# Kernel optimization log

Measured on AMD Instinct MI355X. Metric: run time of the kernel, lower is better.

## Reference

```python
import jax, jax.numpy as jnp
import numpy as np

DIM = 4096
N_HEADS = 32
N_KV = 8
HEAD_DIM = 128
WINDOW = 4096
BSZ = 1
SEQ = 2048
REPEATS = N_HEADS // N_KV
SCALE = HEAD_DIM ** -0.5
NEG_INF = -1e9


def setup_inputs() -> dict:
    key = jax.random.key(0)
    ks = jax.random.split(key, 5)
    x = jax.random.normal(ks[0], (1, BSZ, SEQ, DIM), jnp.float32)
    wq = jax.random.normal(ks[1], (N_HEADS * HEAD_DIM, DIM), jnp.float32) * (DIM ** -0.5)
    wk = jax.random.normal(ks[2], (N_KV * HEAD_DIM, DIM), jnp.float32) * (DIM ** -0.5)
    wv = jax.random.normal(ks[3], (N_KV * HEAD_DIM, DIM), jnp.float32) * (DIM ** -0.5)
    wo = jax.random.normal(ks[4], (DIM, N_HEADS * HEAD_DIM), jnp.float32) * (DIM ** -0.5)
    # rotary frequencies (Mistral/LLaMA style, base 10000)
    inv = 1.0 / (10000.0 ** (np.arange(0, HEAD_DIM, 2, dtype=np.float32) / HEAD_DIM))
    ang = np.outer(np.arange(SEQ, dtype=np.float32), inv)  # [SEQ, HEAD_DIM//2]
    freqs_cos = jnp.asarray(np.cos(ang), jnp.float32)
    freqs_sin = jnp.asarray(np.sin(ang), jnp.float32)
    positions = jnp.arange(SEQ, dtype=jnp.int32)
    # sliding-window causal additive mask [SEQ, SEQ]
    i = np.arange(SEQ)[:, None]
    j = np.arange(SEQ)[None, :]
    allowed = (j <= i) & (j > i - WINDOW)
    mask = jnp.asarray(np.where(allowed, 0.0, NEG_INF).astype(np.float32))
    cache_k = jnp.zeros((BSZ, WINDOW, N_KV, HEAD_DIM), jnp.float32)
    cache_v = jnp.zeros((BSZ, WINDOW, N_KV, HEAD_DIM), jnp.float32)
    return dict(x=x, wq=wq, wk=wk, wv=wv, wo=wo, freqs_cos=freqs_cos,
                freqs_sin=freqs_sin, positions=positions, mask=mask,
                cache_k=cache_k, cache_v=cache_v)


def _rope(x, cos, sin):
    # x: [b, s, h, hd]; pairs (x0,x1),(x2,x3),... treated as complex numbers
    xr = x[..., 0::2]
    xi = x[..., 1::2]
    c = cos[None, :, None, :]
    s = sin[None, :, None, :]
    out_r = xr * c - xi * s
    out_i = xr * s + xi * c
    return jnp.stack([out_r, out_i], axis=-1).reshape(x.shape)


def reference(x, wq, wk, wv, wo, freqs_cos, freqs_sin, positions, mask, cache_k, cache_v):
    b, s = BSZ, SEQ
    xf = x.reshape(b, s, DIM)
    xq = (xf @ wq.T).reshape(b, s, N_HEADS, HEAD_DIM)
    xk = (xf @ wk.T).reshape(b, s, N_KV, HEAD_DIM)
    xv = (xf @ wv.T).reshape(b, s, N_KV, HEAD_DIM)
    xq = _rope(xq, freqs_cos, freqs_sin)
    xk = _rope(xk, freqs_cos, freqs_sin)
    # sliding-window KV cache scatter update (last WINDOW positions, mod WINDOW)
    pos = positions[-WINDOW:] % WINDOW
    cache_k = cache_k.at[:, pos].set(xk[:, -WINDOW:])
    cache_v = cache_v.at[:, pos].set(xv[:, -WINDOW:])
    # prefill branch (positions.shape[0] > 1): attend over current xk/xv
    key = jnp.repeat(xk, REPEATS, axis=2)  # GQA repeat_kv -> [b, s, H, hd]
    val = jnp.repeat(xv, REPEATS, axis=2)
    q = xq.transpose(0, 2, 1, 3)  # [b, H, s, hd]
    k = key.transpose(0, 2, 1, 3)
    v = val.transpose(0, 2, 1, 3)
    scores = jnp.einsum('bhqd,bhkd->bhqk', q, k) * SCALE + mask[None, None]
    probs = jax.nn.softmax(scores, axis=-1)
    out = jnp.einsum('bhqk,bhkd->bhqd', probs, v)
    out = out.transpose(0, 2, 1, 3).reshape(1, b, s, N_HEADS * HEAD_DIM)
    return out @ wo.T, cache_k, cache_v
```

## Files before the change

### kernel.cpp

```cpp
#include <hip/hip_runtime.h>
#include <hip/hip_bf16.h>


typedef __attribute__((ext_vector_type(8))) short short8_t;
typedef __attribute__((ext_vector_type(2))) unsigned uint2_t;
typedef __attribute__((ext_vector_type(8))) __bf16 bf16x8;
typedef __attribute__((ext_vector_type(4))) float f32x4;
typedef __attribute__((ext_vector_type(16))) float f32x16;

#define SEQLEN 2048
#define QSCALE 0.08838834764831845f

__device__ __forceinline__ short f2b(float f) {
  if (!__builtin_isfinite(f)) f = 0.0f;
  union { float f; unsigned u; } v; v.f = f;
  unsigned r = (v.u + 0x7fffu + ((v.u >> 16) & 1u)) >> 16;
  return (short)r;
}
__device__ __forceinline__ float sf(float f) {
  return __builtin_isfinite(f) ? f : 0.0f;
}
__device__ __forceinline__ short8_t cvt8(const float* p) {
  f32x4 a = *(const f32x4*)p;
  f32x4 b = *(const f32x4*)(p + 4);
  short8_t o;
  o[0] = f2b(a[0]); o[1] = f2b(a[1]); o[2] = f2b(a[2]); o[3] = f2b(a[3]);
  o[4] = f2b(b[0]); o[5] = f2b(b[1]); o[6] = f2b(b[2]); o[7] = f2b(b[3]);
  return o;
}
__device__ __forceinline__ unsigned pkb(float lo, float hi) {
  union { float f; unsigned u; } a, b; a.f = lo; b.f = hi;
  unsigned ra = (a.u + 0x7fffu + ((a.u >> 16) & 1u)) >> 16;
  unsigned rb = (b.u + 0x7fffu + ((b.u >> 16) & 1u)) & 0xffff0000u;
  return rb | ra;
}

#define GLD16(gp, lp) __builtin_amdgcn_global_load_lds( \
    (const __attribute__((address_space(1))) void*)(gp), \
    (__attribute__((address_space(3))) void*)(lp), 16, 0, 0)

__global__ __launch_bounds__(256) void cvt_bf16(
    const float* __restrict__ in, short* __restrict__ out)
{
  size_t i = ((size_t)blockIdx.x * 256 + threadIdx.x) * 8;
  *(short8_t*)&out[i] = cvt8(in + i);
}

__global__ __launch_bounds__(256) void gemm_bf(
    const short* __restrict__ A, const short* __restrict__ W,
    float* __restrict__ C1, float* __restrict__ C2,
    int K, int ldc, int splitN)
{
  __shared__ short As[128 * 64];
  __shared__ short Ws[128 * 64];
  const int tid  = threadIdx.x;
  const int lane = tid & 63;
  const int wid  = tid >> 6;
  const int l15  = lane & 15;
  const int l4   = lane >> 4;

  const int nwg = (int)(gridDim.x * gridDim.y);
  int bid = (int)(blockIdx.y * gridDim.x + blockIdx.x);
  int swz = (bid & 7) * (nwg >> 3) + (bid >> 3);
  const int m0 = (swz / (int)gridDim.x) * 128;
  const int n0 = (swz % (int)gridDim.x) * 128;

  const int wr = (wid >> 1) * 64;
  const int wc = (wid & 1) * 64;
  const int srow = tid >> 3;
  const int scol = (tid & 7) * 8;

  f32x4 acc[4][4] = {};

  const short* Ab = A + (size_t)(m0 + srow) * K + scol;
  const short* Wb = W + (size_t)(n0 + srow) * K + scol;

  for (int k0 = 0; k0 < K; k0 += 64) {
#pragma unroll
    for (int i = 0; i < 4; ++i) {
      GLD16(Ab + (size_t)(i * 32) * K + k0, &As[(i * 32 + wid * 8) * 64]);
      GLD16(Wb + (size_t)(i * 32) * K + k0, &Ws[(i * 32 + wid * 8) * 64]);
    }
    __syncthreads();

#pragma unroll
    for (int kk = 0; kk < 2; ++kk) {
      bf16x8 af[4], wf[4];
#pragma unroll
      for (int m = 0; m < 4; ++m)
        af[m] = *(const bf16x8*)&As[(wr + m * 16 + l15) * 64 + kk * 32 + l4 * 8];
#pragma unroll
      for (int n = 0; n < 4; ++n)
        wf[n] = *(const bf16x8*)&Ws[(wc + n * 16 + l15) * 64 + kk * 32 + l4 * 8];
#pragma unroll
      for (int m = 0; m < 4; ++m)
#pragma unroll
        for (int n = 0; n < 4; ++n)
          acc[m][n] = __builtin_amdgcn_mfma_f32_16x16x32_bf16(af[m], wf[n], acc[m][n], 0, 0, 0);
    }
    __syncthreads();
  }

  float* Cb = (n0 < splitN) ? C1 : (C2 - splitN);
#pragma unroll
  for (int m = 0; m < 4; ++m) {
    int rbase = m0 + wr + m * 16 + l4 * 4;
#pragma unroll
    for (int n = 0; n < 4; ++n) {
      int cbase = n0 + wc + n * 16 + l15;
#pragma unroll
      for (int r = 0; r < 4; ++r)
        Cb[(size_t)(rbase + r) * ldc + cbase] = sf(acc[m][n][r]);
    }
  }
}

__device__ __forceinline__ void rope8(const float* in, float* out,
                                      const float* fc, const float* fs, int t, int p0)
{
  f32x4 a = *(const f32x4*)in;
  f32x4 b = *(const f32x4*)(in + 4);
  f32x4 cv = *(const f32x4*)&fc[t * 64 + p0];
  f32x4 sv = *(const f32x4*)&fs[t * 64 + p0];
  float x0[8] = {a[0], a[1], a[2], a[3], b[0], b[1], b[2], b[3]};
#pragma unroll
  for (int i = 0; i < 4; ++i) {
    float xr = x0[2 * i], xi = x0[2 * i + 1];
    out[2 * i]     = sf(xr * cv[i] - xi * sv[i]);
    out[2 * i + 1] = sf(xr * sv[i] + xi * cv[i]);
  }
}

__global__ __launch_bounds__(256) void rope_q_bf(
    const float* __restrict__ q, short* __restrict__ qb,
    const float* __restrict__ fc, const float* __restrict__ fs)
{
  size_t idx = ((size_t)blockIdx.x * 256 + threadIdx.x) * 8;
  int t   = (int)(idx >> 12);
  int col = (int)(idx & 4095);
  float o[8];
  rope8(&q[idx], o, fc, fs, t, (col & 127) >> 1);
  short8_t ob;
#pragma unroll
  for (int i = 0; i < 8; ++i) ob[i] = f2b(o[i] * QSCALE);
  *(short8_t*)&qb[idx] = ob;
}

__global__ __launch_bounds__(256) void rope_k_dual(
    float* __restrict__ ck, short* __restrict__ kb,
    const float* __restrict__ fc, const float* __restrict__ fs)
{
  size_t idx = ((size_t)blockIdx.x * 256 + threadIdx.x) * 8;
  int t   = (int)(idx >> 10);
  int col = (int)(idx & 1023);
  float o[8];
  rope8(&ck[idx], o, fc, fs, t, (col & 127) >> 1);
  *(f32x4*)&ck[idx]     = f32x4{o[0], o[1], o[2], o[3]};
  *(f32x4*)&ck[idx + 4] = f32x4{o[4], o[5], o[6], o[7]};
  short8_t ob;
#pragma unroll
  for (int i = 0; i < 8; ++i) ob[i] = f2b(o[i]);
  *(short8_t*)&kb[idx] = ob;
}

__global__ __launch_bounds__(256) void transpose_v(
    const float* __restrict__ cv, short* __restrict__ Vt)
{
  __shared__ short tile[64][72];
  const int t0 = blockIdx.x * 64;
  const int d0 = blockIdx.y * 64;
  const int h  = blockIdx.z;
  const int tid = threadIdx.x;
  const int r = tid >> 3;
  const int c = (tid & 7) * 8;
#pragma unroll
  for (int it = 0; it < 2; ++it) {
    short8_t v = cvt8(&cv[(size_t)(t0 + it * 32 + r) * 1024 + h * 128 + d0 + c]);
    *(short8_t*)&tile[it * 32 + r][c] = v;
  }
  __syncthreads();
#pragma unroll
  for (int it = 0; it < 2; ++it) {
    int dr = it * 32 + r;
    short8_t v;
#pragma unroll
    for (int i = 0; i < 8; ++i) v[i] = tile[c + i][dr];
    *(short8_t*)&Vt[(size_t)(h * 128 + d0 + dr) * SEQLEN + t0 + c] = v;
  }
}

__global__ __launch_bounds__(64) void attn_fwd3(
    const short* __restrict__ Q,
    const short* __restrict__ Kc,
    const short* __restrict__ Vt,
    short* __restrict__ O)
{
  const int bid = (int)blockIdx.x;
  const int kvh = bid & 7;
  const int j   = bid >> 3;
  const int h   = kvh * 4 + (j & 3);
  const int i   = j >> 2;
  const int qtA = 63 - i, qtB = i;
  const int lane = threadIdx.x & 63;
  const int l31 = lane & 31;
  const int hi  = lane >> 5;

  __shared__ short PA[32][88], PB[32][88];
  __shared__ float exch[64];

  const int q0A = qtA * 32, q0B = qtB * 32;
  const int qgA = q0A + l31, qgB = q0B + l31;
  const int kendA = q0A + 32, kendB = q0B + 32;

  bf16x8 qfA[8], qfB[8];
  {
    const short* qpA = Q + (size_t)qgA * 4096 + h * 128 + hi * 8;
    const short* qpB = Q + (size_t)qgB * 4096 + h * 128 + hi * 8;
#pragma unroll
    for (int ks = 0; ks < 8; ++ks) {
      qfA[ks] = *(const bf16x8*)(qpA + ks * 16);
      qfB[ks] = *(const bf16x8*)(qpB + ks * 16);
    }
  }

  f32x16 oA0 = {}, oA1 = {}, oA2 = {}, oA3 = {};
  f32x16 oB0 = {}, oB1 = {}, oB2 = {}, oB3 = {};
  float mA = -1e30f, lA = 0.f, mB = -1e30f, lB = 0.f;

  for (int kt = 0; kt < kendA; kt += 64) {
    const bool actB = (kt < kendB);
    f32x16 sA0 = {}, sA1 = {}, sB0 = {}, sB1 = {};
    {
      const short* kp = Kc + (size_t)(kt + l31) * 1024 + kvh * 128 + hi * 8;
      __builtin_amdgcn_s_setprio(1);
      if (actB) {
#pragma unroll
        for (int ks = 0; ks < 8; ++ks) {
          bf16x8 k0 = *(const bf16x8*)(kp + ks * 16);
          bf16x8 k1 = *(const bf16x8*)(kp + 32 * 1024 + ks * 16);
          sA0 = __builtin_amdgcn_mfma_f32_32x32x16_bf16(k0, qfA[ks], sA0, 0, 0, 0);
          sA1 = __builtin_amdgcn_mfma_f32_32x32x16_bf16(k1, qfA[ks], sA1, 0, 0, 0);
          sB0 = __builtin_amdgcn_mfma_f32_32x32x16_bf16(k0, qfB[ks], sB0, 0, 0, 0);
          sB1 = __builtin_amdgcn_mfma_f32_32x32x16_bf16(k1, qfB[ks], sB1, 0, 0, 0);
        }
      } else {
#pragma unroll
        for (int ks = 0; ks < 8; ++ks) {
          bf16x8 k0 = *(const bf16x8*)(kp + ks * 16);
          bf16x8 k1 = *(const bf16x8*)(kp + 32 * 1024 + ks * 16);
          sA0 = __builtin_amdgcn_mfma_f32_32x32x16_bf16(k0, qfA[ks], sA0, 0, 0, 0);
          sA1 = __builtin_amdgcn_mfma_f32_32x32x16_bf16(k1, qfA[ks], sA1, 0, 0, 0);
        }
      }
      __builtin_amdgcn_s_setprio(0);
    }

    if (kt + 63 > q0A) {
#pragma unroll
      for (int r = 0; r < 16; ++r) {
        int crow = (r & 3) + 8 * (r >> 2) + 4 * hi;
        if (kt + crow > qgA)      sA0[r] = -1e30f;
        if (kt + 32 + crow > qgA) sA1[r] = -1e30f;
      }
    }
    {
      float t[8];
#pragma unroll
      for (int r = 0; r < 8; ++r)
        t[r] = fmaxf(fmaxf(sA0[r], sA0[r + 8]), fmaxf(sA1[r], sA1[r + 8]));
      float pmax = fmaxf(fmaxf(fmaxf(t[0], t[1]), fmaxf(t[2], t[3])),
                         fmaxf(fmaxf(t[4], t[5]), fmaxf(t[6], t[7])));
      pmax = fmaxf(pmax, __shfl_xor(pmax, 32, 64));
      if (!__all(pmax <= mA + 8.f)) {
        float mnew = fmaxf(mA, pmax);
        float resc = __expf(mA - mnew);
        mA = mnew; lA *= resc;
        if (lane < 32) exch[l31] = resc;
#pragma unroll
        for (int r = 0; r < 16; ++r) {
          float rs = exch[(r & 3) + 8 * (r >> 2) + 4 * hi];
          oA0[r] *= rs; oA1[r] *= rs; oA2[r] *= rs; oA3[r] *= rs;
        }
      }
      float psum = 0.f;
#pragma unroll
      for (int r = 0; r < 16; ++r) { sA0[r] = __expf(sA0[r] - mA); psum += sA0[r]; }
#pragma unroll
      for (int r = 0; r < 16; ++r) { sA1[r] = __expf(sA1[r] - mA); psum += sA1[r]; }
      lA += psum + __shfl_xor(psum, 32, 64);
#pragma unroll
      for (int t4 = 0; t4 < 4; ++t4) {
        int c = 8 * t4 + 4 * hi;
        *(uint2_t*)&PA[l31][c]      = uint2_t{pkb(sA0[4*t4], sA0[4*t4+1]), pkb(sA0[4*t4+2], sA0[4*t4+3])};
        *(uint2_t*)&PA[l31][32 + c] = uint2_t{pkb(sA1[4*t4], sA1[4*t4+1]), pkb(sA1[4*t4+2], sA1[4*t4+3])};
      }
    }

    if (actB) {
      if (kt + 63 > q0B) {
#pragma unroll
        for (int r = 0; r < 16; ++r) {
          int crow = (r & 3) + 8 * (r >> 2) + 4 * hi;
          if (kt + crow > qgB)      sB0[r] = -1e30f;
          if (kt + 32 + crow > qgB) sB1[r] = -1e30f;
        }
      }
      float t[8];
#pragma unroll
      for (int r = 0; r < 8; ++r)
        t[r] = fmaxf(fmaxf(sB0[r], sB0[r + 8]), fmaxf(sB1[r], sB1[r + 8]));
      float pmax = fmaxf(fmaxf(fmaxf(t[0], t[1]), fmaxf(t[2], t[3])),
                         fmaxf(fmaxf(t[4], t[5]), fmaxf(t[6], t[7])));
      pmax = fmaxf(pmax, __shfl_xor(pmax, 32, 64));
      if (!__all(pmax <= mB + 8.f)) {
        float mnew = fmaxf(mB, pmax);
        float resc = __expf(mB - mnew);
        mB = mnew; lB *= resc;
        if (lane < 32) exch[32 + l31] = resc;
#pragma unroll
        for (int r = 0; r < 16; ++r) {
          float rs = exch[32 + (r & 3) + 8 * (r >> 2) + 4 * hi];
          oB0[r] *= rs; oB1[r] *= rs; oB2[r] *= rs; oB3[r] *= rs;
        }
      }
      float psum = 0.f;
#pragma unroll
      for (int r = 0; r < 16; ++r) { sB0[r] = __expf(sB0[r] - mB); psum += sB0[r]; }
#pragma unroll
      for (int r = 0; r < 16; ++r) { sB1[r] = __expf(sB1[r] - mB); psum += sB1[r]; }
      lB += psum + __shfl_xor(psum, 32, 64);
#pragma unroll
      for (int t4 = 0; t4 < 4; ++t4) {
        int c = 8 * t4 + 4 * hi;
        *(uint2_t*)&PB[l31][c]      = uint2_t{pkb(sB0[4*t4], sB0[4*t4+1]), pkb(sB0[4*t4+2], sB0[4*t4+3])};
        *(uint2_t*)&PB[l31][32 + c] = uint2_t{pkb(sB1[4*t4], sB1[4*t4+1]), pkb(sB1[4*t4+2], sB1[4*t4+3])};
      }
    }

    const short* vb = Vt + (size_t)(kvh * 128 + l31) * SEQLEN + kt + hi * 8;
#pragma unroll
    for (int g = 0; g < 4; ++g) {
      const short* vg = vb + g * 16;
      bf16x8 vf0 = *(const bf16x8*)(vg);
      bf16x8 vf1 = *(const bf16x8*)(vg + 32 * SEQLEN);
      bf16x8 vf2 = *(const bf16x8*)(vg + 64 * SEQLEN);
      bf16x8 vf3 = *(const bf16x8*)(vg + (size_t)96 * SEQLEN);
      bf16x8 pfA = *(const bf16x8*)&PA[l31][g * 16 + hi * 8];
      __builtin_amdgcn_s_setprio(1);
      oA0 = __builtin_amdgcn_mfma_f32_32x32x16_bf16(pfA, vf0, oA0, 0, 0, 0);
      oA1 = __builtin_amdgcn_mfma_f32_32x32x16_bf16(pfA, vf1, oA1, 0, 0, 0);
      oA2 = __builtin_amdgcn_mfma_f32_32x32x16_bf16(pfA, vf2, oA2, 0, 0, 0);
      oA3 = __builtin_amdgcn_mfma_f32_32x32x16_bf16(pfA, vf3, oA3, 0, 0, 0);
      if (actB) {
        bf16x8 pfB = *(const bf16x8*)&PB[l31][g * 16 + hi * 8];
        oB0 = __builtin_amdgcn_mfma_f32_32x32x16_bf16(pfB, vf0, oB0, 0, 0, 0);
        oB1 = __builtin_amdgcn_mfma_f32_32x32x16_bf16(pfB, vf1, oB1, 0, 0, 0);
        oB2 = __builtin_amdgcn_mfma_f32_32x32x16_bf16(pfB, vf2, oB2, 0, 0, 0);
        oB3 = __builtin_amdgcn_mfma_f32_32x32x16_bf16(pfB, vf3, oB3, 0, 0, 0);
      }
      __builtin_amdgcn_s_setprio(0);
    }
  }

  if (lane < 32) { exch[l31] = 1.f / lA; exch[32 + l31] = 1.f / lB; }
#pragma unroll
  for (int r = 0; r < 16; ++r) {
    int crow = (r & 3) + 8 * (r >> 2) + 4 * hi;
    float invA = exch[crow];
    float invB = exch[32 + crow];
    short* obA = O + (size_t)(q0A + crow) * 4096 + h * 128 + l31;
    short* obB = O + (size_t)(q0B + crow) * 4096 + h * 128 + l31;
    obA[0]  = f2b(oA0[r] * invA);
    obA[32] = f2b(oA1[r] * invA);
    obA[64] = f2b(oA2[r] * invA);
    obA[96] = f2b(oA3[r] * invA);
    obB[0]  = f2b(oB0[r] * invB);
    obB[32] = f2b(oB1[r] * invB);
    obB[64] = f2b(oB2[r] * invB);
    obB[96] = f2b(oB3[r] * invB);
  }
}

extern "C" void kernel_launch(void* const* d_in, const int* in_sizes, int n_in,
                              void* d_out, int out_size, void* d_ws, size_t ws_size,
                              hipStream_t stream) {
  const float* x  = (const float*)d_in[0];
  const float* wq = (const float*)d_in[1];
  const float* wk = (const float*)d_in[2];
  const float* wv = (const float*)d_in[3];
  const float* wo = (const float*)d_in[4];
  const float* fc = (const float*)d_in[5];
  const float* fs = (const float*)d_in[6];

  float* out = (float*)d_out;
  float* out_main = out;
  float* cache_k  = out + (size_t)2048 * 4096;
  float* cache_v  = cache_k + (size_t)4096 * 8 * 128;

  const size_t MB_W = 33554432;
  const size_t MB_X = 16777216;
  short* slotA = (short*)d_ws;
  short* x_bf  = (short*)((char*)d_ws + MB_W);
  short* attn_out = x_bf;
  short* Vt    = (short*)((char*)d_ws + MB_W + MB_X);
  short* q_bf  = slotA;
  short* k_bf  = slotA + (size_t)2048 * 4096;

  cvt_bf16<<<4096, 256, 0, stream>>>(x, x_bf);
  cvt_bf16<<<8192, 256, 0, stream>>>(wq, slotA);
  gemm_bf<<<dim3(32, 16), 256, 0, stream>>>(x_bf, slotA, out_main, out_main, 4096, 4096, 1 << 30);
  cvt_bf16<<<2048, 256, 0, stream>>>(wk, slotA);
  cvt_bf16<<<2048, 256, 0, stream>>>(wv, slotA + (size_t)1024 * 4096);
  gemm_bf<<<dim3(16, 16), 256, 0, stream>>>(x_bf, slotA, cache_k, cache_v, 4096, 1024, 1024);

  rope_q_bf<<<4096, 256, 0, stream>>>(out_main, q_bf, fc, fs);
  rope_k_dual<<<1024, 256, 0, stream>>>(cache_k, k_bf, fc, fs);
  transpose_v<<<dim3(32, 2, 8), 256, 0, stream>>>(cache_v, Vt);
  hipMemsetAsync(cache_k + (size_t)2048 * 1024, 0, (size_t)2048 * 1024 * 4, stream);
  hipMemsetAsync(cache_v + (size_t)2048 * 1024, 0, (size_t)2048 * 1024 * 4, stream);

  attn_fwd3<<<1024, 64, 0, stream>>>(q_bf, k_bf, Vt, attn_out);

  cvt_bf16<<<8192, 256, 0, stream>>>(wo, slotA);
  gemm_bf<<<dim3(32, 16), 256, 0, stream>>>(attn_out, slotA, out_main, out_main, 4096, 4096, 1 << 30);
}
```

Before: 489.8 us.

## Split attention KV loop across two waves with final softmax merge

The attention kernel now runs two wavefronts per block, each processing alternating 64-key tiles of the same query pair, then merges their running max/sum and output accumulators through shared memory before writing. This halves the serial KV loop length per block and adds wave-level parallelism to hide latency in the long causal rows. In exchange it adds LDS traffic, several block barriers in the merge epilogue, and per-wave duplicated Q registers that may affect occupancy.

```diff
diff --git a/kernel.cpp b/kernel.cpp
--- a/kernel.cpp
+++ b/kernel.cpp
@@ -189,7 +189,7 @@
   }
 }
 
-__global__ __launch_bounds__(64) void attn_fwd3(
+__global__ __launch_bounds__(128, 2) void attn_fwd4(
     const short* __restrict__ Q,
     const short* __restrict__ Kc,
     const short* __restrict__ Vt,
@@ -201,12 +201,17 @@
   const int h   = kvh * 4 + (j & 3);
   const int i   = j >> 2;
   const int qtA = 63 - i, qtB = i;
-  const int lane = threadIdx.x & 63;
+  const int tid = (int)threadIdx.x;
+  const int wid = tid >> 6;
+  const int lane = tid & 63;
   const int l31 = lane & 31;
   const int hi  = lane >> 5;
 
-  __shared__ short PA[32][88], PB[32][88];
-  __shared__ float exch[64];
+  __shared__ short PA[2][32][88], PB[2][32][88];
+  __shared__ float oxch[16][64];
+  __shared__ float mlx[2][2][32][2];
+  __shared__ float scx[2][2][32];
+  __shared__ float rexch[2][64];
 
   const int q0A = qtA * 32, q0B = qtB * 32;
   const int qgA = q0A + l31, qgB = q0B + l31;
@@ -227,7 +232,7 @@
   f32x16 oB0 = {}, oB1 = {}, oB2 = {}, oB3 = {};
   float mA = -1e30f, lA = 0.f, mB = -1e30f, lB = 0.f;
 
-  for (int kt = 0; kt < kendA; kt += 64) {
+  for (int kt = wid * 64; kt < kendA; kt += 128) {
     const bool actB = (kt < kendB);
     f32x16 sA0 = {}, sA1 = {}, sB0 = {}, sB1 = {};
     {
@@ -275,10 +280,10 @@
         float mnew = fmaxf(mA, pmax);
         float resc = __expf(mA - mnew);
         mA = mnew; lA *= resc;
-        if (lane < 32) exch[l31] = resc;
+        if (lane < 32) rexch[wid][l31] = resc;
 #pragma unroll
         for (int r = 0; r < 16; ++r) {
-          float rs = exch[(r & 3) + 8 * (r >> 2) + 4 * hi];
+          float rs = rexch[wid][(r & 3) + 8 * (r >> 2) + 4 * hi];
           oA0[r] *= rs; oA1[r] *= rs; oA2[r] *= rs; oA3[r] *= rs;
         }
       }
@@ -291,8 +296,8 @@
 #pragma unroll
       for (int t4 = 0; t4 < 4; ++t4) {
         int c = 8 * t4 + 4 * hi;
-        *(uint2_t*)&PA[l31][c]      = uint2_t{pkb(sA0[4*t4], sA0[4*t4+1]), pkb(sA0[4*t4+2], sA0[4*t4+3])};
-        *(uint2_t*)&PA[l31][32 + c] = uint2_t{pkb(sA1[4*t4], sA1[4*t4+1]), pkb(sA1[4*t4+2], sA1[4*t4+3])};
+        *(uint2_t*)&PA[wid][l31][c]      = uint2_t{pkb(sA0[4*t4], sA0[4*t4+1]), pkb(sA0[4*t4+2], sA0[4*t4+3])};
+        *(uint2_t*)&PA[wid][l31][32 + c] = uint2_t{pkb(sA1[4*t4], sA1[4*t4+1]), pkb(sA1[4*t4+2], sA1[4*t4+3])};
       }
     }
 
@@ -316,10 +321,10 @@
         float mnew = fmaxf(mB, pmax);
         float resc = __expf(mB - mnew);
         mB = mnew; lB *= resc;
-        if (lane < 32) exch[32 + l31] = resc;
+        if (lane < 32) rexch[wid][32 + l31] = resc;
 #pragma unroll
         for (int r = 0; r < 16; ++r) {
-          float rs = exch[32 + (r & 3) + 8 * (r >> 2) + 4 * hi];
+          float rs = rexch[wid][32 + (r & 3) + 8 * (r >> 2) + 4 * hi];
           oB0[r] *= rs; oB1[r] *= rs; oB2[r] *= rs; oB3[r] *= rs;
         }
       }
@@ -332,8 +337,8 @@
 #pragma unroll
       for (int t4 = 0; t4 < 4; ++t4) {
         int c = 8 * t4 + 4 * hi;
-        *(uint2_t*)&PB[l31][c]      = uint2_t{pkb(sB0[4*t4], sB0[4*t4+1]), pkb(sB0[4*t4+2], sB0[4*t4+3])};
-        *(uint2_t*)&PB[l31][32 + c] = uint2_t{pkb(sB1[4*t4], sB1[4*t4+1]), pkb(sB1[4*t4+2], sB1[4*t4+3])};
+        *(uint2_t*)&PB[wid][l31][c]      = uint2_t{pkb(sB0[4*t4], sB0[4*t4+1]), pkb(sB0[4*t4+2], sB0[4*t4+3])};
+        *(uint2_t*)&PB[wid][l31][32 + c] = uint2_t{pkb(sB1[4*t4], sB1[4*t4+1]), pkb(sB1[4*t4+2], sB1[4*t4+3])};
       }
     }
 
@@ -345,14 +350,14 @@
       bf16x8 vf1 = *(const bf16x8*)(vg + 32 * SEQLEN);
       bf16x8 vf2 = *(const bf16x8*)(vg + 64 * SEQLEN);
       bf16x8 vf3 = *(const bf16x8*)(vg + (size_t)96 * SEQLEN);
-      bf16x8 pfA = *(const bf16x8*)&PA[l31][g * 16 + hi * 8];
+      bf16x8 pfA = *(const bf16x8*)&PA[wid][l31][g * 16 + hi * 8];
       __builtin_amdgcn_s_setprio(1);
       oA0 = __builtin_amdgcn_mfma_f32_32x32x16_bf16(pfA, vf0, oA0, 0, 0, 0);
       oA1 = __builtin_amdgcn_mfma_f32_32x32x16_bf16(pfA, vf1, oA1, 0, 0, 0);
       oA2 = __builtin_amdgcn_mfma_f32_32x32x16_bf16(pfA, vf2, oA2, 0, 0, 0);
       oA3 = __builtin_amdgcn_mfma_f32_32x32x16_bf16(pfA, vf3, oA3, 0, 0, 0);
       if (actB) {
-        bf16x8 pfB = *(const bf16x8*)&PB[l31][g * 16 + hi * 8];
+        bf16x8 pfB = *(const bf16x8*)&PB[wid][l31][g * 16 + hi * 8];
         oB0 = __builtin_amdgcn_mfma_f32_32x32x16_bf16(pfB, vf0, oB0, 0, 0, 0);
         oB1 = __builtin_amdgcn_mfma_f32_32x32x16_bf16(pfB, vf1, oB1, 0, 0, 0);
         oB2 = __builtin_amdgcn_mfma_f32_32x32x16_bf16(pfB, vf2, oB2, 0, 0, 0);
@@ -362,23 +367,52 @@
     }
   }
 
-  if (lane < 32) { exch[l31] = 1.f / lA; exch[32 + l31] = 1.f / lB; }
-#pragma unroll
-  for (int r = 0; r < 16; ++r) {
-    int crow = (r & 3) + 8 * (r >> 2) + 4 * hi;
-    float invA = exch[crow];
-    float invB = exch[32 + crow];
-    short* obA = O + (size_t)(q0A + crow) * 4096 + h * 128 + l31;
-    short* obB = O + (size_t)(q0B + crow) * 4096 + h * 128 + l31;
-    obA[0]  = f2b(oA0[r] * invA);
-    obA[32] = f2b(oA1[r] * invA);
-    obA[64] = f2b(oA2[r] * invA);
-    obA[96] = f2b(oA3[r] * invA);
-    obB[0]  = f2b(oB0[r] * invB);
-    obB[32] = f2b(oB1[r] * invB);
-    obB[64] = f2b(oB2[r] * invB);
-    obB[96] = f2b(oB3[r] * invB);
-  }
+  if (lane < 32) {
+    mlx[wid][0][l31][0] = mA; mlx[wid][0][l31][1] = lA;
+    mlx[wid][1][l31][0] = mB; mlx[wid][1][l31][1] = lB;
+  }
+  __syncthreads();
+  if (wid == 0 && lane < 32) {
+#pragma unroll
+    for (int T = 0; T < 2; ++T) {
+      float m0 = mlx[0][T][l31][0], l0 = mlx[0][T][l31][1];
+      float m1 = mlx[1][T][l31][0], l1 = mlx[1][T][l31][1];
+      float M  = fmaxf(m0, m1);
+      float e0 = __expf(m0 - M), e1 = __expf(m1 - M);
+      float den = l0 * e0 + l1 * e1;
+      scx[0][T][l31] = e0 / den;
+      scx[1][T][l31] = e1 / den;
+    }
+  }
+  __syncthreads();
+
+#define MERGE_STORE(oreg, T, q0, g) do {                                     \
+    if (wid == 1) {                                                          \
+      _Pragma("unroll")                                                      \
+      for (int r = 0; r < 16; ++r)                                           \
+        oxch[r][lane] = (oreg)[r] * scx[1][T][(r & 3) + 8 * (r >> 2) + 4 * hi]; \
+    }                                                                        \
+    __syncthreads();                                                         \
+    if (wid == 0) {                                                          \
+      _Pragma("unroll")                                                      \
+      for (int r = 0; r < 16; ++r) {                                         \
+        int crow = (r & 3) + 8 * (r >> 2) + 4 * hi;                          \
+        float v = (oreg)[r] * scx[0][T][crow] + oxch[r][lane];               \
+        O[(size_t)((q0) + crow) * 4096 + h * 128 + (g) * 32 + l31] = f2b(v); \
+      }                                                                      \
+    }                                                                        \
+    __syncthreads();                                                         \
+  } while (0)
+
+  MERGE_STORE(oA0, 0, q0A, 0);
+  MERGE_STORE(oA1, 0, q0A, 1);
+  MERGE_STORE(oA2, 0, q0A, 2);
+  MERGE_STORE(oA3, 0, q0A, 3);
+  MERGE_STORE(oB0, 1, q0B, 0);
+  MERGE_STORE(oB1, 1, q0B, 1);
+  MERGE_STORE(oB2, 1, q0B, 2);
+  MERGE_STORE(oB3, 1, q0B, 3);
+#undef MERGE_STORE
 }
 
 extern "C" void kernel_launch(void* const* d_in, const int* in_sizes, int n_in,
@@ -419,7 +453,7 @@
   hipMemsetAsync(cache_k + (size_t)2048 * 1024, 0, (size_t)2048 * 1024 * 4, stream);
   hipMemsetAsync(cache_v + (size_t)2048 * 1024, 0, (size_t)2048 * 1024 * 4, stream);
 
-  attn_fwd3<<<1024, 64, 0, stream>>>(q_bf, k_bf, Vt, attn_out);
+  attn_fwd4<<<1024, 128, 0, stream>>>(q_bf, k_bf, Vt, attn_out);
 
   cvt_bf16<<<8192, 256, 0, stream>>>(wo, slotA);
   gemm_bf<<<dim3(32, 16), 256, 0, stream>>>(attn_out, slotA, out_main, out_main, 4096, 4096, 1 << 30);
```

After: 492.8 us. About the same (+0.6%).

## Share K/V tiles in LDS across the four query heads of a KV group

Applied to the files above, without the earlier changes.

The attention kernel now uses 256-thread blocks whose four waves each handle one of the four query heads sharing a KV head. K and V tiles are loaded cooperatively into LDS with an XOR swizzle and reused by all four waves, instead of each single-wave block reading K and V straight from global memory. This cuts redundant global and L2 traffic for K and V by up to four times, at the cost of two block barriers per key tile and fewer, larger blocks (256 instead of 1024).

```diff
diff --git a/kernel.cpp b/kernel.cpp
--- a/kernel.cpp
+++ b/kernel.cpp
@@ -189,7 +189,7 @@
   }
 }
 
-__global__ __launch_bounds__(64) void attn_fwd3(
+__global__ __launch_bounds__(256) void attn_fwd5(
     const short* __restrict__ Q,
     const short* __restrict__ Kc,
     const short* __restrict__ Vt,
@@ -197,16 +197,19 @@
 {
   const int bid = (int)blockIdx.x;
   const int kvh = bid & 7;
-  const int j   = bid >> 3;
-  const int h   = kvh * 4 + (j & 3);
-  const int i   = j >> 2;
+  const int i   = bid >> 3;
   const int qtA = 63 - i, qtB = i;
-  const int lane = threadIdx.x & 63;
+  const int tid = (int)threadIdx.x;
+  const int wid = tid >> 6;
+  const int h   = kvh * 4 + wid;
+  const int lane = tid & 63;
   const int l31 = lane & 31;
   const int hi  = lane >> 5;
 
-  __shared__ short PA[32][88], PB[32][88];
-  __shared__ float exch[64];
+  __shared__ short Ks[64 * 128];
+  __shared__ short Vs[128 * 64];
+  __shared__ short PA[4][32][72], PB[4][32][72];
+  __shared__ float exch[4][64];
 
   const int q0A = qtA * 32, q0B = qtB * 32;
   const int qgA = q0A + l31, qgB = q0B + l31;
@@ -227,29 +230,40 @@
   f32x16 oB0 = {}, oB1 = {}, oB2 = {}, oB3 = {};
   float mA = -1e30f, lA = 0.f, mB = -1e30f, lB = 0.f;
 
+  const int krow_base = wid * 16;
+  const int vrow_base = wid * 32;
+
   for (int kt = 0; kt < kendA; kt += 64) {
+#pragma unroll
+    for (int it = 0; it < 4; ++it) {
+      int krow = krow_base + it * 4 + (lane >> 4);
+      int kchp = lane & 15;
+      int kgch = kchp ^ (krow & 15);
+      GLD16(Kc + (size_t)(kt + krow) * 1024 + kvh * 128 + kgch * 8,
+            &Ks[wid * 2048 + it * 512]);
+      int vrow = vrow_base + it * 8 + (lane >> 3);
+      int vchp = lane & 7;
+      int vgch = vchp ^ (vrow & 7);
+      GLD16(Vt + (size_t)(kvh * 128 + vrow) * SEQLEN + kt + vgch * 8,
+            &Vs[wid * 2048 + it * 512]);
+    }
+    __syncthreads();
+
     const bool actB = (kt < kendB);
     f32x16 sA0 = {}, sA1 = {}, sB0 = {}, sB1 = {};
     {
-      const short* kp = Kc + (size_t)(kt + l31) * 1024 + kvh * 128 + hi * 8;
+      const int xk = l31 & 15;
       __builtin_amdgcn_s_setprio(1);
-      if (actB) {
-#pragma unroll
-        for (int ks = 0; ks < 8; ++ks) {
-          bf16x8 k0 = *(const bf16x8*)(kp + ks * 16);
-          bf16x8 k1 = *(const bf16x8*)(kp + 32 * 1024 + ks * 16);
-          sA0 = __builtin_amdgcn_mfma_f32_32x32x16_bf16(k0, qfA[ks], sA0, 0, 0, 0);
-          sA1 = __builtin_amdgcn_mfma_f32_32x32x16_bf16(k1, qfA[ks], sA1, 0, 0, 0);
+#pragma unroll
+      for (int ks = 0; ks < 8; ++ks) {
+        int ch = (ks * 2 + hi) ^ xk;
+        bf16x8 k0 = *(const bf16x8*)&Ks[l31 * 128 + ch * 8];
+        bf16x8 k1 = *(const bf16x8*)&Ks[(32 + l31) * 128 + ch * 8];
+        sA0 = __builtin_amdgcn_mfma_f32_32x32x16_bf16(k0, qfA[ks], sA0, 0, 0, 0);
+        sA1 = __builtin_amdgcn_mfma_f32_32x32x16_bf16(k1, qfA[ks], sA1, 0, 0, 0);
+        if (actB) {
           sB0 = __builtin_amdgcn_mfma_f32_32x32x16_bf16(k0, qfB[ks], sB0, 0, 0, 0);
           sB1 = __builtin_amdgcn_mfma_f32_32x32x16_bf16(k1, qfB[ks], sB1, 0, 0, 0);
-        }
-      } else {
-#pragma unroll
-        for (int ks = 0; ks < 8; ++ks) {
-          bf16x8 k0 = *(const bf16x8*)(kp + ks * 16);
-          bf16x8 k1 = *(const bf16x8*)(kp + 32 * 1024 + ks * 16);
-          sA0 = __builtin_amdgcn_mfma_f32_32x32x16_bf16(k0, qfA[ks], sA0, 0, 0, 0);
-          sA1 = __builtin_amdgcn_mfma_f32_32x32x16_bf16(k1, qfA[ks], sA1, 0, 0, 0);
         }
       }
       __builtin_amdgcn_s_setprio(0);
@@ -275,10 +289,10 @@
         float mnew = fmaxf(mA, pmax);
         float resc = __expf(mA - mnew);
         mA = mnew; lA *= resc;
-        if (lane < 32) exch[l31] = resc;
+        if (lane < 32) exch[wid][l31] = resc;
 #pragma unroll
         for (int r = 0; r < 16; ++r) {
-          float rs = exch[(r & 3) + 8 * (r >> 2) + 4 * hi];
+          float rs = exch[wid][(r & 3) + 8 * (r >> 2) + 4 * hi];
           oA0[r] *= rs; oA1[r] *= rs; oA2[r] *= rs; oA3[r] *= rs;
         }
       }
@@ -291,8 +305,8 @@
 #pragma unroll
       for (int t4 = 0; t4 < 4; ++t4) {
         int c = 8 * t4 + 4 * hi;
-        *(uint2_t*)&PA[l31][c]      = uint2_t{pkb(sA0[4*t4], sA0[4*t4+1]), pkb(sA0[4*t4+2], sA0[4*t4+3])};
-        *(uint2_t*)&PA[l31][32 + c] = uint2_t{pkb(sA1[4*t4], sA1[4*t4+1]), pkb(sA1[4*t4+2], sA1[4*t4+3])};
+        *(uint2_t*)&PA[wid][l31][c]      = uint2_t{pkb(sA0[4*t4], sA0[4*t4+1]), pkb(sA0[4*t4+2], sA0[4*t4+3])};
+        *(uint2_t*)&PA[wid][l31][32 + c] = uint2_t{pkb(sA1[4*t4], sA1[4*t4+1]), pkb(sA1[4*t4+2], sA1[4*t4+3])};
       }
     }
 
@@ -316,10 +330,10 @@
         float mnew = fmaxf(mB, pmax);
         float resc = __expf(mB - mnew);
         mB = mnew; lB *= resc;
-        if (lane < 32) exch[32 + l31] = resc;
+        if (lane < 32) exch[wid][32 + l31] = resc;
 #pragma unroll
         for (int r = 0; r < 16; ++r) {
-          float rs = exch[32 + (r & 3) + 8 * (r >> 2) + 4 * hi];
+          float rs = exch[wid][32 + (r & 3) + 8 * (r >> 2) + 4 * hi];
           oB0[r] *= rs; oB1[r] *= rs; oB2[r] *= rs; oB3[r] *= rs;
         }
       }
@@ -332,42 +346,45 @@
 #pragma unroll
       for (int t4 = 0; t4 < 4; ++t4) {
         int c = 8 * t4 + 4 * hi;
-        *(uint2_t*)&PB[l31][c]      = uint2_t{pkb(sB0[4*t4], sB0[4*t4+1]), pkb(sB0[4*t4+2], sB0[4*t4+3])};
-        *(uint2_t*)&PB[l31][32 + c] = uint2_t{pkb(sB1[4*t4], sB1[4*t4+1]), pkb(sB1[4*t4+2], sB1[4*t4+3])};
-      }
-    }
-
-    const short* vb = Vt + (size_t)(kvh * 128 + l31) * SEQLEN + kt + hi * 8;
-#pragma unroll
-    for (int g = 0; g < 4; ++g) {
-      const short* vg = vb + g * 16;
-      bf16x8 vf0 = *(const bf16x8*)(vg);
-      bf16x8 vf1 = *(const bf16x8*)(vg + 32 * SEQLEN);
-      bf16x8 vf2 = *(const bf16x8*)(vg + 64 * SEQLEN);
-      bf16x8 vf3 = *(const bf16x8*)(vg + (size_t)96 * SEQLEN);
-      bf16x8 pfA = *(const bf16x8*)&PA[l31][g * 16 + hi * 8];
-      __builtin_amdgcn_s_setprio(1);
-      oA0 = __builtin_amdgcn_mfma_f32_32x32x16_bf16(pfA, vf0, oA0, 0, 0, 0);
-      oA1 = __builtin_amdgcn_mfma_f32_32x32x16_bf16(pfA, vf1, oA1, 0, 0, 0);
-      oA2 = __builtin_amdgcn_mfma_f32_32x32x16_bf16(pfA, vf2, oA2, 0, 0, 0);
-      oA3 = __builtin_amdgcn_mfma_f32_32x32x16_bf16(pfA, vf3, oA3, 0, 0, 0);
-      if (actB) {
-        bf16x8 pfB = *(const bf16x8*)&PB[l31][g * 16 + hi * 8];
-        oB0 = __builtin_amdgcn_mfma_f32_32x32x16_bf16(pfB, vf0, oB0, 0, 0, 0);
-        oB1 = __builtin_amdgcn_mfma_f32_32x32x16_bf16(pfB, vf1, oB1, 0, 0, 0);
-        oB2 = __builtin_amdgcn_mfma_f32_32x32x16_bf16(pfB, vf2, oB2, 0, 0, 0);
-        oB3 = __builtin_amdgcn_mfma_f32_32x32x16_bf16(pfB, vf3, oB3, 0, 0, 0);
-      }
-      __builtin_amdgcn_s_setprio(0);
-    }
-  }
-
-  if (lane < 32) { exch[l31] = 1.f / lA; exch[32 + l31] = 1.f / lB; }
+        *(uint2_t*)&PB[wid][l31][c]      = uint2_t{pkb(sB0[4*t4], sB0[4*t4+1]), pkb(sB0[4*t4+2], sB0[4*t4+3])};
+        *(uint2_t*)&PB[wid][l31][32 + c] = uint2_t{pkb(sB1[4*t4], sB1[4*t4+1]), pkb(sB1[4*t4+2], sB1[4*t4+3])};
+      }
+    }
+
+    {
+      const int xv = l31 & 7;
+#pragma unroll
+      for (int g = 0; g < 4; ++g) {
+        int ch = (g * 2 + hi) ^ xv;
+        bf16x8 vf0 = *(const bf16x8*)&Vs[(l31)       * 64 + ch * 8];
+        bf16x8 vf1 = *(const bf16x8*)&Vs[(32 + l31)  * 64 + ch * 8];
+        bf16x8 vf2 = *(const bf16x8*)&Vs[(64 + l31)  * 64 + ch * 8];
+        bf16x8 vf3 = *(const bf16x8*)&Vs[(96 + l31)  * 64 + ch * 8];
+        bf16x8 pfA = *(const bf16x8*)&PA[wid][l31][g * 16 + hi * 8];
+        __builtin_amdgcn_s_setprio(1);
+        oA0 = __builtin_amdgcn_mfma_f32_32x32x16_bf16(pfA, vf0, oA0, 0, 0, 0);
+        oA1 = __builtin_amdgcn_mfma_f32_32x32x16_bf16(pfA, vf1, oA1, 0, 0, 0);
+        oA2 = __builtin_amdgcn_mfma_f32_32x32x16_bf16(pfA, vf2, oA2, 0, 0, 0);
+        oA3 = __builtin_amdgcn_mfma_f32_32x32x16_bf16(pfA, vf3, oA3, 0, 0, 0);
+        if (actB) {
+          bf16x8 pfB = *(const bf16x8*)&PB[wid][l31][g * 16 + hi * 8];
+          oB0 = __builtin_amdgcn_mfma_f32_32x32x16_bf16(pfB, vf0, oB0, 0, 0, 0);
+          oB1 = __builtin_amdgcn_mfma_f32_32x32x16_bf16(pfB, vf1, oB1, 0, 0, 0);
+          oB2 = __builtin_amdgcn_mfma_f32_32x32x16_bf16(pfB, vf2, oB2, 0, 0, 0);
+          oB3 = __builtin_amdgcn_mfma_f32_32x32x16_bf16(pfB, vf3, oB3, 0, 0, 0);
+        }
+        __builtin_amdgcn_s_setprio(0);
+      }
+    }
+    __syncthreads();
+  }
+
+  if (lane < 32) { exch[wid][l31] = 1.f / lA; exch[wid][32 + l31] = 1.f / lB; }
 #pragma unroll
   for (int r = 0; r < 16; ++r) {
     int crow = (r & 3) + 8 * (r >> 2) + 4 * hi;
-    float invA = exch[crow];
-    float invB = exch[32 + crow];
+    float invA = exch[wid][crow];
+    float invB = exch[wid][32 + crow];
     short* obA = O + (size_t)(q0A + crow) * 4096 + h * 128 + l31;
     short* obB = O + (size_t)(q0B + crow) * 4096 + h * 128 + l31;
     obA[0]  = f2b(oA0[r] * invA);
@@ -419,7 +436,7 @@
   hipMemsetAsync(cache_k + (size_t)2048 * 1024, 0, (size_t)2048 * 1024 * 4, stream);
   hipMemsetAsync(cache_v + (size_t)2048 * 1024, 0, (size_t)2048 * 1024 * 4, stream);
 
-  attn_fwd3<<<1024, 64, 0, stream>>>(q_bf, k_bf, Vt, attn_out);
+  attn_fwd5<<<256, 256, 0, stream>>>(q_bf, k_bf, Vt, attn_out);
 
   cvt_bf16<<<8192, 256, 0, stream>>>(wo, slotA);
   gemm_bf<<<dim3(32, 16), 256, 0, stream>>>(attn_out, slotA, out_main, out_main, 4096, 4096, 1 << 30);
```

New measurement: 452.2 us. 7.7% less time.
